# Optimization experiments

Measured on AMD Instinct MI355X. Metric: run time of the kernel, lower is better.

The kernel has to match this reference:

```python
import jax, jax.numpy as jnp
import numpy as np

B, L, V, D = 8, 2048, 1024, 512  # batch, seq (max_len), vocab_size (input feat), embedding_dim

def setup_inputs() -> dict:
    key = jax.random.key(0)
    kx, kq, kk, kv = jax.random.split(key, 4)
    scale = 1.0 / np.sqrt(V)
    return {
        "x": jax.random.normal(kx, (B, L, V), dtype=jnp.float32),
        "Wq": jax.random.uniform(kq, (D, V), dtype=jnp.float32, minval=-scale, maxval=scale),
        "Wk": jax.random.uniform(kk, (D, V), dtype=jnp.float32, minval=-scale, maxval=scale),
        "Wv": jax.random.uniform(kv, (D, V), dtype=jnp.float32, minval=-scale, maxval=scale),
    }

def reference(x, Wq, Wk, Wv):
    # nn.Linear without bias: y = x @ W.T
    q = jnp.einsum('blv,dv->bld', x, Wq)
    k = jnp.einsum('blv,dv->bld', x, Wk)
    v = jnp.einsum('blv,dv->bld', x, Wv)
    scores = jnp.einsum('bqd,bkd->bqk', q, k) / jnp.sqrt(jnp.float32(D))
    attn = jax.nn.softmax(scores, axis=2)
    return jnp.einsum('bqk,bkd->bqd', attn, v)
```

## Files before the change

### kernel.cpp

```cpp
#include <hip/hip_runtime.h>
#include <cstdint>
#include <cstddef>


typedef __attribute__((ext_vector_type(8))) __bf16 bf16x8;
typedef __attribute__((ext_vector_type(4))) float f32x4;
typedef __attribute__((ext_vector_type(4))) unsigned short ushort4v;
typedef __attribute__((ext_vector_type(4))) unsigned int uint4v;

__device__ __forceinline__ unsigned short f2bf(float f) {
  unsigned u = __float_as_uint(f);
  return (unsigned short)((u + 0x7fffu + ((u >> 16) & 1u)) >> 16);
}

__device__ __forceinline__ void async_load16(const unsigned short* g, unsigned short* l) {
  __builtin_amdgcn_global_load_lds(
      (__attribute__((address_space(1))) void*)(g),
      (__attribute__((address_space(3))) void*)(l), 16, 0, 0);
}

__global__ __launch_bounds__(256) void cvt_all(
    const float* __restrict__ x, const float* __restrict__ Wq,
    const float* __restrict__ Wk, const float* __restrict__ Wv,
    unsigned short* __restrict__ xb, unsigned short* __restrict__ wf) {
  int u0 = blockIdx.x, tid = threadIdx.x;
  const float* src;
  unsigned short* dst;
  int i;
  if (u0 < 16384) {
    i = (u0 * 256 + tid) * 4;
    src = x; dst = xb;
  } else {
    int bx = u0 - 16384;
    src = (bx < 512) ? Wq : (bx < 1024) ? Wk : Wv;
    int seg = (bx < 512) ? 0 : (bx < 1024) ? 1 : 2;
    i = ((bx & 511) * 256 + tid) * 4;
    dst = wf + seg * 524288;
  }
  float4 v = *(const float4*)(src + i);
  ushort4v o;
  o.x = f2bf(v.x); o.y = f2bf(v.y); o.z = f2bf(v.z); o.w = f2bf(v.w);
  *(ushort4v*)(dst + i) = o;
}

template <int NT, bool RSUM>
__device__ __forceinline__ void core8p(
    const unsigned short* __restrict__ A, const unsigned short* __restrict__ B,
    int ldA, int ldB, unsigned short* smem, int tid,
    f32x4 (&acc)[4][4], float (&rsum)[4]) {
  const int lane = tid & 63, wid = tid >> 6;
  const int wm = wid & 3, wn = wid >> 2;
  const int cl = lane & 15, g = lane >> 4;
  const int r0 = tid >> 3;
  const int cs8 = ((tid & 7) ^ (r0 & 7)) * 8;

  #pragma unroll
  for (int p = 0; p < 4; ++p)
    async_load16(&A[(size_t)(p * 64 + r0) * ldA + cs8], &smem[(p * 512 + tid) * 8]);
  #pragma unroll
  for (int p = 0; p < 2; ++p)
    async_load16(&B[(size_t)(p * 64 + r0) * ldB + cs8], &smem[16384 + (p * 512 + tid) * 8]);
  #pragma unroll
  for (int p = 0; p < 4; ++p)
    async_load16(&A[(size_t)(p * 64 + r0) * ldA + 64 + cs8], &smem[24576 + (p * 512 + tid) * 8]);
  #pragma unroll
  for (int p = 0; p < 2; ++p)
    async_load16(&B[(size_t)(p * 64 + r0) * ldB + 64 + cs8], &smem[40960 + (p * 512 + tid) * 8]);
  asm volatile("s_waitcnt vmcnt(6)" ::: "memory");
  __builtin_amdgcn_s_barrier();

  int cur = 0;
  for (int t = 0; t < NT; ++t) {
    unsigned short* bufc = smem + cur * 24576;
    int nb = cur + 2; if (nb >= 3) nb -= 3;
    unsigned short* bufn = smem + nb * 24576;
    const bool st = (t + 2 < NT);
    const int k2 = (t + 2) * 64;

    #pragma unroll
    for (int kh = 0; kh < 2; ++kh) {
      bf16x8 a4[4], b4[4];
      #pragma unroll
      for (int mt = 0; mt < 4; ++mt) {
        int rr = wm * 64 + mt * 16 + cl;
        a4[mt] = *(const bf16x8*)&bufc[(rr * 8 + ((kh * 4 + g) ^ (rr & 7))) * 8];
      }
      #pragma unroll
      for (int nt = 0; nt < 4; ++nt) {
        int rr = wn * 64 + nt * 16 + cl;
        b4[nt] = *(const bf16x8*)&bufc[16384 + (rr * 8 + ((kh * 4 + g) ^ (rr & 7))) * 8];
      }
      if (kh == 0) {
        if (st) {
          #pragma unroll
          for (int p = 0; p < 4; ++p)
            async_load16(&A[(size_t)(p * 64 + r0) * ldA + k2 + cs8],
                         &bufn[(p * 512 + tid) * 8]);
        }
      } else {
        if (st) {
          #pragma unroll
          for (int p = 0; p < 2; ++p)
            async_load16(&B[(size_t)(p * 64 + r0) * ldB + k2 + cs8],
                         &bufn[16384 + (p * 512 + tid) * 8]);
          asm volatile("s_waitcnt vmcnt(6)" ::: "memory");
        } else if (t + 1 < NT) {
          asm volatile("s_waitcnt vmcnt(0)" ::: "memory");
        }
      }
      __builtin_amdgcn_s_barrier();
      asm volatile("s_waitcnt lgkmcnt(0)" ::: "memory");
      __builtin_amdgcn_sched_barrier(0);
      if (RSUM) {
        #pragma unroll
        for (int nt = 0; nt < 4; ++nt) {
          uint4v u = __builtin_bit_cast(uint4v, b4[nt]);
          #pragma unroll
          for (int q = 0; q < 4; ++q)
            rsum[nt] += __uint_as_float(u[q] << 16) +
                        __uint_as_float(u[q] & 0xffff0000u);
        }
      }
      __builtin_amdgcn_s_setprio(1);
      #pragma unroll
      for (int mt = 0; mt < 4; ++mt)
        #pragma unroll
        for (int nt = 0; nt < 4; ++nt)
          acc[mt][nt] = __builtin_amdgcn_mfma_f32_16x16x32_bf16(
              a4[mt], b4[nt], acc[mt][nt], 0, 0, 0);
      __builtin_amdgcn_s_setprio(0);
      __builtin_amdgcn_s_barrier();
    }
    cur = cur + 1; if (cur == 3) cur = 0;
  }
}

__global__ __launch_bounds__(512, 2) void gemm_qkv8(
    const unsigned short* __restrict__ A0,
    const unsigned short* __restrict__ Bw,
    unsigned short* __restrict__ qk,
    unsigned short* __restrict__ vT) {
  extern __shared__ __align__(16) unsigned short smem[];
  const int tid = threadIdx.x;
  int flat = blockIdx.x;
  int sub = flat >> 3;
  int bxp = sub % 12;
  int byp = (flat & 7) * 8 + sub / 12;
  const unsigned short* A = A0 + (size_t)byp * 256 * 1024;
  const unsigned short* B = Bw + (size_t)bxp * 128 * 1024;

  f32x4 acc[4][4] = {};
  float rsum[4];
  core8p<16, false>(A, B, 1024, 1024, smem, tid, acc, rsum);

  const int lane = tid & 63, wid = tid >> 6;
  const int wm = wid & 3, wn = wid >> 2, cl = lane & 15, g = lane >> 4;

  if (bxp < 8) {
    unsigned short* Cc = qk + (size_t)byp * 256 * 1024 + (size_t)bxp * 128;
    #pragma unroll
    for (int mt = 0; mt < 4; ++mt)
      #pragma unroll
      for (int nt = 0; nt < 4; ++nt) {
        int col = wn * 64 + nt * 16 + cl;
        int row0 = wm * 64 + mt * 16 + g * 4;
        #pragma unroll
        for (int j = 0; j < 4; ++j)
          Cc[(size_t)(row0 + j) * 1024 + col] = f2bf(acc[mt][nt][j]);
      }
  } else {
    int nvx = bxp - 8;
    #pragma unroll
    for (int mt = 0; mt < 4; ++mt)
      #pragma unroll
      for (int nt = 0; nt < 4; ++nt) {
        int d = nvx * 128 + wn * 64 + nt * 16 + cl;
        int grow0 = byp * 256 + wm * 64 + mt * 16 + g * 4;
        int b = grow0 >> 11, l0 = grow0 & 2047;
        ushort4v o;
        o.x = f2bf(acc[mt][nt][0]); o.y = f2bf(acc[mt][nt][1]);
        o.z = f2bf(acc[mt][nt][2]); o.w = f2bf(acc[mt][nt][3]);
        *(ushort4v*)&vT[(size_t)b * 1048576 + (size_t)d * 2048 + l0] = o;
      }
  }
}

__global__ __launch_bounds__(512, 2) void gemm_pvT8(
    const unsigned short* __restrict__ S, const unsigned short* __restrict__ vT,
    float* __restrict__ out) {
  extern __shared__ __align__(16) unsigned short smem[];
  const int tid = threadIdx.x;
  int flat = blockIdx.x;
  int b = flat & 7, rem = flat >> 3;
  int dblk = rem & 1, qblk = rem >> 1;
  const unsigned short* A  = vT + (size_t)b * 1048576 + (size_t)dblk * 256 * 2048;
  const unsigned short* Bs = S  + (size_t)b * 4194304 + (size_t)qblk * 128 * 2048;

  f32x4 acc[4][4] = {};
  float rsum[4] = {0.f, 0.f, 0.f, 0.f};
  core8p<32, true>(A, Bs, 2048, 2048, smem, tid, acc, rsum);

  const int lane = tid & 63, wid = tid >> 6;
  const int wm = wid & 3, wn = wid >> 2, cl = lane & 15, g = lane >> 4;

  #pragma unroll
  for (int nt = 0; nt < 4; ++nt) {
    float v = rsum[nt];
    v += __shfl_xor(v, 16, 64);
    v += __shfl_xor(v, 32, 64);
    rsum[nt] = v;
  }

  #pragma unroll
  for (int nt = 0; nt < 4; ++nt) {
    float inv = __builtin_amdgcn_rcpf(rsum[nt]);
    int qpos = qblk * 128 + wn * 64 + nt * 16 + cl;
    #pragma unroll
    for (int mt = 0; mt < 4; ++mt) {
      int d0 = dblk * 256 + wm * 64 + mt * 16 + g * 4;
      float* op = out + ((size_t)b * 2048 + qpos) * 512 + d0;
      float4 o;
      o.x = acc[mt][nt][0] * inv;
      o.y = acc[mt][nt][1] * inv;
      o.z = acc[mt][nt][2] * inv;
      o.w = acc[mt][nt][3] * inv;
      *(float4*)op = o;
    }
  }
}

__global__ __launch_bounds__(256) void gemm_exp(
    const unsigned short* __restrict__ qk,
    unsigned short* __restrict__ S) {
  const float scale = 0.044194173824159216f;
  __shared__ unsigned short sA[128 * 64];
  __shared__ unsigned short sB[128 * 64];
  const int tid = threadIdx.x;
  const int lane = tid & 63, wid = tid >> 6;
  const int wm = wid & 1, wn = wid >> 1;
  const int cl = lane & 15, g = lane >> 4;

  int flat = blockIdx.x + (blockIdx.y << 4) + (blockIdx.z << 8);
  int z = flat & 7, rem = flat >> 3;
  int bxp = rem & 15, byp = rem >> 4;

  const unsigned short* A  = qk + (size_t)z * 2097152 + (size_t)byp * 128 * 1024;
  const unsigned short* Bk = qk + 512 + (size_t)z * 2097152 + (size_t)bxp * 128 * 1024;

  f32x4 acc[4][4] = {};

  for (int k0 = 0; k0 < 512; k0 += 64) {
    __syncthreads();
    #pragma unroll
    for (int p = 0; p < 4; ++p) {
      int u = p * 256 + tid;
      int r = u >> 3, cs = (u & 7) ^ (r & 7);
      async_load16(&A[(size_t)r * 1024 + k0 + cs * 8], &sA[u * 8]);
      async_load16(&Bk[(size_t)r * 1024 + k0 + cs * 8], &sB[u * 8]);
    }
    __syncthreads();

    bf16x8 aF[4][2], bF[4][2];
    #pragma unroll
    for (int t = 0; t < 4; ++t)
      #pragma unroll
      for (int kh = 0; kh < 2; ++kh) {
        int ra = wm * 64 + t * 16 + cl;
        aF[t][kh] = *(const bf16x8*)&sA[(ra * 8 + ((kh * 4 + g) ^ (ra & 7))) * 8];
        int rb = wn * 64 + t * 16 + cl;
        bF[t][kh] = *(const bf16x8*)&sB[(rb * 8 + ((kh * 4 + g) ^ (rb & 7))) * 8];
      }
    #pragma unroll
    for (int mt = 0; mt < 4; ++mt)
      #pragma unroll
      for (int nt = 0; nt < 4; ++nt)
        #pragma unroll
        for (int kh = 0; kh < 2; ++kh)
          acc[mt][nt] = __builtin_amdgcn_mfma_f32_16x16x32_bf16(
              aF[mt][kh], bF[nt][kh], acc[mt][nt], 0, 0, 0);
  }

  unsigned short* Cc = S + (size_t)z * 4194304 +
                       (size_t)byp * 128 * 2048 + (size_t)bxp * 128;
  #pragma unroll
  for (int mt = 0; mt < 4; ++mt)
    #pragma unroll
    for (int nt = 0; nt < 4; ++nt) {
      int col = wn * 64 + nt * 16 + cl;
      int row0 = wm * 64 + mt * 16 + g * 4;
      #pragma unroll
      for (int j = 0; j < 4; ++j)
        Cc[(size_t)(row0 + j) * 2048 + col] =
            f2bf(__expf(acc[mt][nt][j] * scale));
    }
}

extern "C" void kernel_launch(void* const* d_in, const int* in_sizes, int n_in,
                              void* d_out, int out_size, void* d_ws, size_t ws_size,
                              hipStream_t stream) {
  const float* x  = (const float*)d_in[0];
  const float* Wq = (const float*)d_in[1];
  const float* Wk = (const float*)d_in[2];
  const float* Wv = (const float*)d_in[3];
  float* out = (float*)d_out;
  char* ws = (char*)d_ws;

  unsigned short* xb = (unsigned short*)ws;
  unsigned short* S  = (unsigned short*)ws;
  unsigned short* wf = (unsigned short*)(ws + 33554432);
  unsigned short* qk = (unsigned short*)(ws + 67108864);
  unsigned short* vT = (unsigned short*)(ws + 100663296);

  static bool inited = false;
  if (!inited) {
    hipFuncSetAttribute((const void*)gemm_qkv8,
                        hipFuncAttributeMaxDynamicSharedMemorySize, 147456);
    hipFuncSetAttribute((const void*)gemm_pvT8,
                        hipFuncAttributeMaxDynamicSharedMemorySize, 147456);
    inited = true;
  }

  hipLaunchKernelGGL(cvt_all, dim3(17920), dim3(256), 0, stream,
                     x, Wq, Wk, Wv, xb, wf);

  hipLaunchKernelGGL(gemm_qkv8, dim3(768), dim3(512), 147456, stream,
                     xb, wf, qk, vT);

  hipLaunchKernelGGL(gemm_exp, dim3(16, 16, 8), dim3(256), 0, stream, qk, S);

  hipLaunchKernelGGL(gemm_pvT8, dim3(256), dim3(512), 147456, stream,
                     S, vT, out);

  (void)in_sizes; (void)n_in; (void)out_size; (void)ws_size;
}
```

Baseline: 268.3 us.

## Rewrite QKV GEMM with 4-wave blocks and larger per-wave tiles; grid-stride convert

Replaces the 8-wave shared core QKV projection GEMM with a dedicated 4-wave kernel in which each wave computes a 128x64 tile (8x4 MFMAs). Loads are triple-buffered with explicit vmcnt/lgkmcnt waits and sched barriers. The aim is more MFMA work per LDS fragment read and less cross-wave synchronisation. The fp32-to-bf16 convert kernel becomes grid-stride over 2048 blocks instead of launching 17920. The cost is higher register pressure at one block per CU with 144KB of LDS, which leaves fewer waves to hide latency.

```diff
diff --git a/kernel.cpp b/kernel.cpp
--- a/kernel.cpp
+++ b/kernel.cpp
@@ -23,24 +23,149 @@
     const float* __restrict__ x, const float* __restrict__ Wq,
     const float* __restrict__ Wk, const float* __restrict__ Wv,
     unsigned short* __restrict__ xb, unsigned short* __restrict__ wf) {
-  int u0 = blockIdx.x, tid = threadIdx.x;
-  const float* src;
-  unsigned short* dst;
-  int i;
-  if (u0 < 16384) {
-    i = (u0 * 256 + tid) * 4;
-    src = x; dst = xb;
+  int tid = threadIdx.x;
+  for (int u0 = blockIdx.x; u0 < 17920; u0 += 2048) {
+    const float* src;
+    unsigned short* dst;
+    int i;
+    if (u0 < 16384) {
+      i = (u0 * 256 + tid) * 4;
+      src = x; dst = xb;
+    } else {
+      int bx = u0 - 16384;
+      src = (bx < 512) ? Wq : (bx < 1024) ? Wk : Wv;
+      int seg = (bx < 512) ? 0 : (bx < 1024) ? 1 : 2;
+      i = ((bx & 511) * 256 + tid) * 4;
+      dst = wf + seg * 524288;
+    }
+    float4 v = *(const float4*)(src + i);
+    ushort4v o;
+    o.x = f2bf(v.x); o.y = f2bf(v.y); o.z = f2bf(v.z); o.w = f2bf(v.w);
+    *(ushort4v*)(dst + i) = o;
+  }
+}
+
+__global__ __launch_bounds__(256, 1) void gemm_qkv4(
+    const unsigned short* __restrict__ A0,
+    const unsigned short* __restrict__ Bw,
+    unsigned short* __restrict__ qk,
+    unsigned short* __restrict__ vT) {
+  extern __shared__ __align__(16) unsigned short smem[];
+  const int tid = threadIdx.x;
+  const int lane = tid & 63, wid = tid >> 6;
+  const int wm = wid & 1, wn = wid >> 1;
+  const int cl = lane & 15, g = lane >> 4;
+  const int r0 = tid >> 3;
+  const int cs8 = ((tid & 7) ^ (r0 & 7)) * 8;
+
+  int flat = blockIdx.x;
+  int sub = flat >> 3;
+  int bxp = sub % 12;
+  int byp = (flat & 7) * 8 + sub / 12;
+
+  const unsigned short* A = A0 + (size_t)byp * 256 * 1024;
+  const unsigned short* B = Bw + (size_t)bxp * 128 * 1024;
+
+  f32x4 acc[8][4] = {};
+
+  #pragma unroll
+  for (int p = 0; p < 8; ++p)
+    async_load16(&A[(size_t)(p * 32 + r0) * 1024 + cs8], &smem[(p * 256 + tid) * 8]);
+  #pragma unroll
+  for (int p = 0; p < 4; ++p)
+    async_load16(&B[(size_t)(p * 32 + r0) * 1024 + cs8], &smem[16384 + (p * 256 + tid) * 8]);
+  #pragma unroll
+  for (int p = 0; p < 8; ++p)
+    async_load16(&A[(size_t)(p * 32 + r0) * 1024 + 64 + cs8], &smem[24576 + (p * 256 + tid) * 8]);
+  #pragma unroll
+  for (int p = 0; p < 4; ++p)
+    async_load16(&B[(size_t)(p * 32 + r0) * 1024 + 64 + cs8], &smem[40960 + (p * 256 + tid) * 8]);
+  asm volatile("s_waitcnt vmcnt(12)" ::: "memory");
+  __builtin_amdgcn_s_barrier();
+
+  int cur = 0;
+  const int NT = 16;
+  for (int t = 0; t < NT; ++t) {
+    unsigned short* bufc = smem + cur * 24576;
+    int nb = cur + 2; if (nb >= 3) nb -= 3;
+    unsigned short* bufn = smem + nb * 24576;
+    const bool st = (t + 2 < NT);
+    const int k2 = (t + 2) * 64;
+
+    #pragma unroll
+    for (int kh = 0; kh < 2; ++kh) {
+      bf16x8 a8[8], b4[4];
+      #pragma unroll
+      for (int mt = 0; mt < 8; ++mt) {
+        int rr = wm * 128 + mt * 16 + cl;
+        a8[mt] = *(const bf16x8*)&bufc[(rr * 8 + ((kh * 4 + g) ^ (rr & 7))) * 8];
+      }
+      #pragma unroll
+      for (int nt = 0; nt < 4; ++nt) {
+        int rr = wn * 64 + nt * 16 + cl;
+        b4[nt] = *(const bf16x8*)&bufc[16384 + (rr * 8 + ((kh * 4 + g) ^ (rr & 7))) * 8];
+      }
+      if (kh == 0) {
+        if (st) {
+          #pragma unroll
+          for (int p = 0; p < 8; ++p)
+            async_load16(&A[(size_t)(p * 32 + r0) * 1024 + k2 + cs8],
+                         &bufn[(p * 256 + tid) * 8]);
+        }
+      } else {
+        if (st) {
+          #pragma unroll
+          for (int p = 0; p < 4; ++p)
+            async_load16(&B[(size_t)(p * 32 + r0) * 1024 + k2 + cs8],
+                         &bufn[16384 + (p * 256 + tid) * 8]);
+          asm volatile("s_waitcnt vmcnt(12)" ::: "memory");
+        } else if (t + 1 < NT) {
+          asm volatile("s_waitcnt vmcnt(0)" ::: "memory");
+        }
+      }
+      __builtin_amdgcn_s_barrier();
+      asm volatile("s_waitcnt lgkmcnt(0)" ::: "memory");
+      __builtin_amdgcn_sched_barrier(0);
+      __builtin_amdgcn_s_setprio(1);
+      #pragma unroll
+      for (int mt = 0; mt < 8; ++mt)
+        #pragma unroll
+        for (int nt = 0; nt < 4; ++nt)
+          acc[mt][nt] = __builtin_amdgcn_mfma_f32_16x16x32_bf16(
+              a8[mt], b4[nt], acc[mt][nt], 0, 0, 0);
+      __builtin_amdgcn_s_setprio(0);
+      __builtin_amdgcn_s_barrier();
+    }
+    cur = cur + 1; if (cur == 3) cur = 0;
+  }
+
+  if (bxp < 8) {
+    unsigned short* Cc = qk + (size_t)byp * 256 * 1024 + (size_t)bxp * 128;
+    #pragma unroll
+    for (int mt = 0; mt < 8; ++mt)
+      #pragma unroll
+      for (int nt = 0; nt < 4; ++nt) {
+        int col = wn * 64 + nt * 16 + cl;
+        int row0 = wm * 128 + mt * 16 + g * 4;
+        #pragma unroll
+        for (int j = 0; j < 4; ++j)
+          Cc[(size_t)(row0 + j) * 1024 + col] = f2bf(acc[mt][nt][j]);
+      }
   } else {
-    int bx = u0 - 16384;
-    src = (bx < 512) ? Wq : (bx < 1024) ? Wk : Wv;
-    int seg = (bx < 512) ? 0 : (bx < 1024) ? 1 : 2;
-    i = ((bx & 511) * 256 + tid) * 4;
-    dst = wf + seg * 524288;
-  }
-  float4 v = *(const float4*)(src + i);
-  ushort4v o;
-  o.x = f2bf(v.x); o.y = f2bf(v.y); o.z = f2bf(v.z); o.w = f2bf(v.w);
-  *(ushort4v*)(dst + i) = o;
+    int nvx = bxp - 8;
+    #pragma unroll
+    for (int mt = 0; mt < 8; ++mt)
+      #pragma unroll
+      for (int nt = 0; nt < 4; ++nt) {
+        int d = nvx * 128 + wn * 64 + nt * 16 + cl;
+        int grow0 = byp * 256 + wm * 128 + mt * 16 + g * 4;
+        int b = grow0 >> 11, l0 = grow0 & 2047;
+        ushort4v o;
+        o.x = f2bf(acc[mt][nt][0]); o.y = f2bf(acc[mt][nt][1]);
+        o.z = f2bf(acc[mt][nt][2]); o.w = f2bf(acc[mt][nt][3]);
+        *(ushort4v*)&vT[(size_t)b * 1048576 + (size_t)d * 2048 + l0] = o;
+      }
+  }
 }
 
 template <int NT, bool RSUM>
@@ -135,56 +260,6 @@
   }
 }
 
-__global__ __launch_bounds__(512, 2) void gemm_qkv8(
-    const unsigned short* __restrict__ A0,
-    const unsigned short* __restrict__ Bw,
-    unsigned short* __restrict__ qk,
-    unsigned short* __restrict__ vT) {
-  extern __shared__ __align__(16) unsigned short smem[];
-  const int tid = threadIdx.x;
-  int flat = blockIdx.x;
-  int sub = flat >> 3;
-  int bxp = sub % 12;
-  int byp = (flat & 7) * 8 + sub / 12;
-  const unsigned short* A = A0 + (size_t)byp * 256 * 1024;
-  const unsigned short* B = Bw + (size_t)bxp * 128 * 1024;
-
-  f32x4 acc[4][4] = {};
-  float rsum[4];
-  core8p<16, false>(A, B, 1024, 1024, smem, tid, acc, rsum);
-
-  const int lane = tid & 63, wid = tid >> 6;
-  const int wm = wid & 3, wn = wid >> 2, cl = lane & 15, g = lane >> 4;
-
-  if (bxp < 8) {
-    unsigned short* Cc = qk + (size_t)byp * 256 * 1024 + (size_t)bxp * 128;
-    #pragma unroll
-    for (int mt = 0; mt < 4; ++mt)
-      #pragma unroll
-      for (int nt = 0; nt < 4; ++nt) {
-        int col = wn * 64 + nt * 16 + cl;
-        int row0 = wm * 64 + mt * 16 + g * 4;
-        #pragma unroll
-        for (int j = 0; j < 4; ++j)
-          Cc[(size_t)(row0 + j) * 1024 + col] = f2bf(acc[mt][nt][j]);
-      }
-  } else {
-    int nvx = bxp - 8;
-    #pragma unroll
-    for (int mt = 0; mt < 4; ++mt)
-      #pragma unroll
-      for (int nt = 0; nt < 4; ++nt) {
-        int d = nvx * 128 + wn * 64 + nt * 16 + cl;
-        int grow0 = byp * 256 + wm * 64 + mt * 16 + g * 4;
-        int b = grow0 >> 11, l0 = grow0 & 2047;
-        ushort4v o;
-        o.x = f2bf(acc[mt][nt][0]); o.y = f2bf(acc[mt][nt][1]);
-        o.z = f2bf(acc[mt][nt][2]); o.w = f2bf(acc[mt][nt][3]);
-        *(ushort4v*)&vT[(size_t)b * 1048576 + (size_t)d * 2048 + l0] = o;
-      }
-  }
-}
-
 __global__ __launch_bounds__(512, 2) void gemm_pvT8(
     const unsigned short* __restrict__ S, const unsigned short* __restrict__ vT,
     float* __restrict__ out) {
@@ -313,17 +388,17 @@
 
   static bool inited = false;
   if (!inited) {
-    hipFuncSetAttribute((const void*)gemm_qkv8,
+    hipFuncSetAttribute((const void*)gemm_qkv4,
                         hipFuncAttributeMaxDynamicSharedMemorySize, 147456);
     hipFuncSetAttribute((const void*)gemm_pvT8,
                         hipFuncAttributeMaxDynamicSharedMemorySize, 147456);
     inited = true;
   }
 
-  hipLaunchKernelGGL(cvt_all, dim3(17920), dim3(256), 0, stream,
+  hipLaunchKernelGGL(cvt_all, dim3(2048), dim3(256), 0, stream,
                      x, Wq, Wk, Wv, xb, wf);
 
-  hipLaunchKernelGGL(gemm_qkv8, dim3(768), dim3(512), 147456, stream,
+  hipLaunchKernelGGL(gemm_qkv4, dim3(768), dim3(256), 147456, stream,
                      xb, wf, qk, vT);
 
   hipLaunchKernelGGL(gemm_exp, dim3(16, 16, 8), dim3(256), 0, stream, qk, S);
```

Result: slower. 282.6 us (+5.3%).

## Replace P·V kernel with 128x128-tile grid and grid-stride the conversion kernel

Applied to the files above, without the earlier changes.

Replaces the large 512-thread, triple-buffered transposed P·V kernel (256 blocks of 256x128 tiles) with a simpler 256-thread kernel that uses 128x128 tiles over P rows and V columns. That doubles the block count to 512 so more of the GPU's compute units get work. Row sums for the softmax normalisation are now taken from the A fragments and reduced through shared memory. The catch is that the new kernel is single-buffered with two barriers per k-step, so load and compute no longer overlap. Separately, the fp32-to-bf16 conversion kernel now launches a fixed 2048 blocks that loop over the work in a grid-stride pattern, instead of one block per chunk.

```diff
diff --git a/kernel.cpp b/kernel.cpp
--- a/kernel.cpp
+++ b/kernel.cpp
@@ -23,31 +23,32 @@
     const float* __restrict__ x, const float* __restrict__ Wq,
     const float* __restrict__ Wk, const float* __restrict__ Wv,
     unsigned short* __restrict__ xb, unsigned short* __restrict__ wf) {
-  int u0 = blockIdx.x, tid = threadIdx.x;
-  const float* src;
-  unsigned short* dst;
-  int i;
-  if (u0 < 16384) {
-    i = (u0 * 256 + tid) * 4;
-    src = x; dst = xb;
-  } else {
-    int bx = u0 - 16384;
-    src = (bx < 512) ? Wq : (bx < 1024) ? Wk : Wv;
-    int seg = (bx < 512) ? 0 : (bx < 1024) ? 1 : 2;
-    i = ((bx & 511) * 256 + tid) * 4;
-    dst = wf + seg * 524288;
-  }
-  float4 v = *(const float4*)(src + i);
-  ushort4v o;
-  o.x = f2bf(v.x); o.y = f2bf(v.y); o.z = f2bf(v.z); o.w = f2bf(v.w);
-  *(ushort4v*)(dst + i) = o;
-}
-
-template <int NT, bool RSUM>
+  int tid = threadIdx.x;
+  for (int u0 = blockIdx.x; u0 < 17920; u0 += 2048) {
+    const float* src;
+    unsigned short* dst;
+    int i;
+    if (u0 < 16384) {
+      i = (u0 * 256 + tid) * 4;
+      src = x; dst = xb;
+    } else {
+      int bx = u0 - 16384;
+      src = (bx < 512) ? Wq : (bx < 1024) ? Wk : Wv;
+      int seg = (bx < 512) ? 0 : (bx < 1024) ? 1 : 2;
+      i = ((bx & 511) * 256 + tid) * 4;
+      dst = wf + seg * 524288;
+    }
+    float4 v = *(const float4*)(src + i);
+    ushort4v o;
+    o.x = f2bf(v.x); o.y = f2bf(v.y); o.z = f2bf(v.z); o.w = f2bf(v.w);
+    *(ushort4v*)(dst + i) = o;
+  }
+}
+
+template <int NT>
 __device__ __forceinline__ void core8p(
     const unsigned short* __restrict__ A, const unsigned short* __restrict__ B,
-    int ldA, int ldB, unsigned short* smem, int tid,
-    f32x4 (&acc)[4][4], float (&rsum)[4]) {
+    int ldA, int ldB, unsigned short* smem, int tid, f32x4 (&acc)[4][4]) {
   const int lane = tid & 63, wid = tid >> 6;
   const int wm = wid & 3, wn = wid >> 2;
   const int cl = lane & 15, g = lane >> 4;
@@ -111,16 +112,6 @@
       __builtin_amdgcn_s_barrier();
       asm volatile("s_waitcnt lgkmcnt(0)" ::: "memory");
       __builtin_amdgcn_sched_barrier(0);
-      if (RSUM) {
-        #pragma unroll
-        for (int nt = 0; nt < 4; ++nt) {
-          uint4v u = __builtin_bit_cast(uint4v, b4[nt]);
-          #pragma unroll
-          for (int q = 0; q < 4; ++q)
-            rsum[nt] += __uint_as_float(u[q] << 16) +
-                        __uint_as_float(u[q] & 0xffff0000u);
-        }
-      }
       __builtin_amdgcn_s_setprio(1);
       #pragma unroll
       for (int mt = 0; mt < 4; ++mt)
@@ -150,8 +141,7 @@
   const unsigned short* B = Bw + (size_t)bxp * 128 * 1024;
 
   f32x4 acc[4][4] = {};
-  float rsum[4];
-  core8p<16, false>(A, B, 1024, 1024, smem, tid, acc, rsum);
+  core8p<16>(A, B, 1024, 1024, smem, tid, acc);
 
   const int lane = tid & 63, wid = tid >> 6;
   const int wm = wid & 3, wn = wid >> 2, cl = lane & 15, g = lane >> 4;
@@ -182,50 +172,6 @@
         o.z = f2bf(acc[mt][nt][2]); o.w = f2bf(acc[mt][nt][3]);
         *(ushort4v*)&vT[(size_t)b * 1048576 + (size_t)d * 2048 + l0] = o;
       }
-  }
-}
-
-__global__ __launch_bounds__(512, 2) void gemm_pvT8(
-    const unsigned short* __restrict__ S, const unsigned short* __restrict__ vT,
-    float* __restrict__ out) {
-  extern __shared__ __align__(16) unsigned short smem[];
-  const int tid = threadIdx.x;
-  int flat = blockIdx.x;
-  int b = flat & 7, rem = flat >> 3;
-  int dblk = rem & 1, qblk = rem >> 1;
-  const unsigned short* A  = vT + (size_t)b * 1048576 + (size_t)dblk * 256 * 2048;
-  const unsigned short* Bs = S  + (size_t)b * 4194304 + (size_t)qblk * 128 * 2048;
-
-  f32x4 acc[4][4] = {};
-  float rsum[4] = {0.f, 0.f, 0.f, 0.f};
-  core8p<32, true>(A, Bs, 2048, 2048, smem, tid, acc, rsum);
-
-  const int lane = tid & 63, wid = tid >> 6;
-  const int wm = wid & 3, wn = wid >> 2, cl = lane & 15, g = lane >> 4;
-
-  #pragma unroll
-  for (int nt = 0; nt < 4; ++nt) {
-    float v = rsum[nt];
-    v += __shfl_xor(v, 16, 64);
-    v += __shfl_xor(v, 32, 64);
-    rsum[nt] = v;
-  }
-
-  #pragma unroll
-  for (int nt = 0; nt < 4; ++nt) {
-    float inv = __builtin_amdgcn_rcpf(rsum[nt]);
-    int qpos = qblk * 128 + wn * 64 + nt * 16 + cl;
-    #pragma unroll
-    for (int mt = 0; mt < 4; ++mt) {
-      int d0 = dblk * 256 + wm * 64 + mt * 16 + g * 4;
-      float* op = out + ((size_t)b * 2048 + qpos) * 512 + d0;
-      float4 o;
-      o.x = acc[mt][nt][0] * inv;
-      o.y = acc[mt][nt][1] * inv;
-      o.z = acc[mt][nt][2] * inv;
-      o.w = acc[mt][nt][3] * inv;
-      *(float4*)op = o;
-    }
   }
 }
 
@@ -295,6 +241,95 @@
     }
 }
 
+__global__ __launch_bounds__(256) void gemm_pv(
+    const unsigned short* __restrict__ P, const unsigned short* __restrict__ vT,
+    float* __restrict__ out) {
+  __shared__ unsigned short sA[128 * 64];
+  __shared__ unsigned short sB[128 * 64];
+  __shared__ float rs[128];
+  const int tid = threadIdx.x;
+  const int lane = tid & 63, wid = tid >> 6;
+  const int wm = wid & 1, wn = wid >> 1;
+  const int cl = lane & 15, g = lane >> 4;
+
+  int flat = blockIdx.x + (blockIdx.y << 2) + (blockIdx.z << 6);
+  int z = flat & 7, rem = flat >> 3;
+  int bxp = rem & 3, byp = rem >> 2;
+
+  const int m0 = byp * 128, n0 = bxp * 128;
+  const unsigned short* A  = P + (size_t)z * 4194304 + (size_t)m0 * 2048;
+  const unsigned short* Bv = vT + (size_t)z * 1048576 + (size_t)n0 * 2048;
+
+  f32x4 acc[4][4] = {};
+  float rsum[4] = {0.f, 0.f, 0.f, 0.f};
+
+  for (int k0 = 0; k0 < 2048; k0 += 64) {
+    __syncthreads();
+    #pragma unroll
+    for (int p = 0; p < 4; ++p) {
+      int u = p * 256 + tid;
+      int r = u >> 3, cs = (u & 7) ^ (r & 7);
+      async_load16(&A[(size_t)r * 2048 + k0 + cs * 8], &sA[u * 8]);
+      async_load16(&Bv[(size_t)r * 2048 + k0 + cs * 8], &sB[u * 8]);
+    }
+    __syncthreads();
+
+    bf16x8 aF[4][2], bF[4][2];
+    #pragma unroll
+    for (int t = 0; t < 4; ++t)
+      #pragma unroll
+      for (int kh = 0; kh < 2; ++kh) {
+        int ra = wm * 64 + t * 16 + cl;
+        aF[t][kh] = *(const bf16x8*)&sA[(ra * 8 + ((kh * 4 + g) ^ (ra & 7))) * 8];
+        int rb = wn * 64 + t * 16 + cl;
+        bF[t][kh] = *(const bf16x8*)&sB[(rb * 8 + ((kh * 4 + g) ^ (rb & 7))) * 8];
+      }
+    #pragma unroll
+    for (int t = 0; t < 4; ++t)
+      #pragma unroll
+      for (int kh = 0; kh < 2; ++kh) {
+        uint4v u = __builtin_bit_cast(uint4v, aF[t][kh]);
+        #pragma unroll
+        for (int q = 0; q < 4; ++q)
+          rsum[t] += __uint_as_float(u[q] << 16) +
+                     __uint_as_float(u[q] & 0xffff0000u);
+      }
+    #pragma unroll
+    for (int mt = 0; mt < 4; ++mt)
+      #pragma unroll
+      for (int nt = 0; nt < 4; ++nt)
+        #pragma unroll
+        for (int kh = 0; kh < 2; ++kh)
+          acc[mt][nt] = __builtin_amdgcn_mfma_f32_16x16x32_bf16(
+              aF[mt][kh], bF[nt][kh], acc[mt][nt], 0, 0, 0);
+  }
+
+  #pragma unroll
+  for (int mt = 0; mt < 4; ++mt) {
+    float v = rsum[mt];
+    v += __shfl_xor(v, 16, 64);
+    v += __shfl_xor(v, 32, 64);
+    if (wn == 0 && lane < 16) rs[wm * 64 + mt * 16 + lane] = v;
+  }
+  __syncthreads();
+
+  #pragma unroll
+  for (int mt = 0; mt < 4; ++mt) {
+    int row0l = wm * 64 + mt * 16 + g * 4;
+    float inv[4];
+    #pragma unroll
+    for (int j = 0; j < 4; ++j) inv[j] = __builtin_amdgcn_rcpf(rs[row0l + j]);
+    #pragma unroll
+    for (int nt = 0; nt < 4; ++nt) {
+      int col = n0 + wn * 64 + nt * 16 + cl;
+      float* op = out + ((size_t)z * 2048 + m0 + row0l) * 512 + col;
+      #pragma unroll
+      for (int j = 0; j < 4; ++j)
+        op[(size_t)j * 512] = acc[mt][nt][j] * inv[j];
+    }
+  }
+}
+
 extern "C" void kernel_launch(void* const* d_in, const int* in_sizes, int n_in,
                               void* d_out, int out_size, void* d_ws, size_t ws_size,
                               hipStream_t stream) {
@@ -315,12 +350,10 @@
   if (!inited) {
     hipFuncSetAttribute((const void*)gemm_qkv8,
                         hipFuncAttributeMaxDynamicSharedMemorySize, 147456);
-    hipFuncSetAttribute((const void*)gemm_pvT8,
-                        hipFuncAttributeMaxDynamicSharedMemorySize, 147456);
     inited = true;
   }
 
-  hipLaunchKernelGGL(cvt_all, dim3(17920), dim3(256), 0, stream,
+  hipLaunchKernelGGL(cvt_all, dim3(2048), dim3(256), 0, stream,
                      x, Wq, Wk, Wv, xb, wf);
 
   hipLaunchKernelGGL(gemm_qkv8, dim3(768), dim3(512), 147456, stream,
@@ -328,8 +361,7 @@
 
   hipLaunchKernelGGL(gemm_exp, dim3(16, 16, 8), dim3(256), 0, stream, qk, S);
 
-  hipLaunchKernelGGL(gemm_pvT8, dim3(256), dim3(512), 147456, stream,
-                     S, vT, out);
+  hipLaunchKernelGGL(gemm_pv, dim3(4, 16, 8), dim3(256), 0, stream, S, vT, out);
 
   (void)in_sizes; (void)n_in; (void)out_size; (void)ws_size;
 }
```

Result: faster. 251.2 us (-6.4%).

## Move QK^T exp onto pipelined 256x128 core and reorient PV GEMM

Applied to the files above, without the earlier changes.

Replaces the simple single-buffered QK^T+exp kernel with one built on the shared multi-stage async-load core8p, using 256x128 tiles and 512 threads. The PV GEMM is reoriented so P is the A operand, with row sums taken from A fragments and shared through LDS for normalization. The conversion kernel becomes grid-stride with fewer blocks. The aim is better latency hiding and MFMA utilization in the score GEMM, at the cost of extra LDS for the row sums and scalar fp32 output stores.

```diff
diff --git a/kernel.cpp b/kernel.cpp
--- a/kernel.cpp
+++ b/kernel.cpp
@@ -23,24 +23,26 @@
     const float* __restrict__ x, const float* __restrict__ Wq,
     const float* __restrict__ Wk, const float* __restrict__ Wv,
     unsigned short* __restrict__ xb, unsigned short* __restrict__ wf) {
-  int u0 = blockIdx.x, tid = threadIdx.x;
-  const float* src;
-  unsigned short* dst;
-  int i;
-  if (u0 < 16384) {
-    i = (u0 * 256 + tid) * 4;
-    src = x; dst = xb;
-  } else {
-    int bx = u0 - 16384;
-    src = (bx < 512) ? Wq : (bx < 1024) ? Wk : Wv;
-    int seg = (bx < 512) ? 0 : (bx < 1024) ? 1 : 2;
-    i = ((bx & 511) * 256 + tid) * 4;
-    dst = wf + seg * 524288;
-  }
-  float4 v = *(const float4*)(src + i);
-  ushort4v o;
-  o.x = f2bf(v.x); o.y = f2bf(v.y); o.z = f2bf(v.z); o.w = f2bf(v.w);
-  *(ushort4v*)(dst + i) = o;
+  int tid = threadIdx.x;
+  for (int u0 = blockIdx.x; u0 < 17920; u0 += 2048) {
+    const float* src;
+    unsigned short* dst;
+    int i;
+    if (u0 < 16384) {
+      i = (u0 * 256 + tid) * 4;
+      src = x; dst = xb;
+    } else {
+      int bx = u0 - 16384;
+      src = (bx < 512) ? Wq : (bx < 1024) ? Wk : Wv;
+      int seg = (bx < 512) ? 0 : (bx < 1024) ? 1 : 2;
+      i = ((bx & 511) * 256 + tid) * 4;
+      dst = wf + seg * 524288;
+    }
+    float4 v = *(const float4*)(src + i);
+    ushort4v o;
+    o.x = f2bf(v.x); o.y = f2bf(v.y); o.z = f2bf(v.z); o.w = f2bf(v.w);
+    *(ushort4v*)(dst + i) = o;
+  }
 }
 
 template <int NT, bool RSUM>
@@ -113,11 +115,11 @@
       __builtin_amdgcn_sched_barrier(0);
       if (RSUM) {
         #pragma unroll
-        for (int nt = 0; nt < 4; ++nt) {
-          uint4v u = __builtin_bit_cast(uint4v, b4[nt]);
+        for (int mt = 0; mt < 4; ++mt) {
+          uint4v u = __builtin_bit_cast(uint4v, a4[mt]);
           #pragma unroll
           for (int q = 0; q < 4; ++q)
-            rsum[nt] += __uint_as_float(u[q] << 16) +
+            rsum[mt] += __uint_as_float(u[q] << 16) +
                         __uint_as_float(u[q] & 0xffff0000u);
         }
       }
@@ -185,114 +187,86 @@
   }
 }
 
-__global__ __launch_bounds__(512, 2) void gemm_pvT8(
-    const unsigned short* __restrict__ S, const unsigned short* __restrict__ vT,
+__global__ __launch_bounds__(512, 2) void gemm_exp8(
+    const unsigned short* __restrict__ qk,
+    unsigned short* __restrict__ S) {
+  const float scale = 0.044194173824159216f;
+  extern __shared__ __align__(16) unsigned short smem[];
+  const int tid = threadIdx.x;
+  int flat = blockIdx.x;
+  int z = flat & 7, rem = flat >> 3;
+  int bxp = rem & 15, byp = rem >> 4;
+
+  const unsigned short* A  = qk + (size_t)z * 2097152 + (size_t)byp * 256 * 1024;
+  const unsigned short* Bk = qk + 512 + (size_t)z * 2097152 + (size_t)bxp * 128 * 1024;
+
+  f32x4 acc[4][4] = {};
+  float rsum[4];
+  core8p<8, false>(A, Bk, 1024, 1024, smem, tid, acc, rsum);
+
+  const int lane = tid & 63, wid = tid >> 6;
+  const int wm = wid & 3, wn = wid >> 2, cl = lane & 15, g = lane >> 4;
+
+  unsigned short* Cc = S + (size_t)z * 4194304 +
+                       (size_t)byp * 256 * 2048 + (size_t)bxp * 128;
+  #pragma unroll
+  for (int mt = 0; mt < 4; ++mt)
+    #pragma unroll
+    for (int nt = 0; nt < 4; ++nt) {
+      int col = wn * 64 + nt * 16 + cl;
+      int row0 = wm * 64 + mt * 16 + g * 4;
+      #pragma unroll
+      for (int j = 0; j < 4; ++j)
+        Cc[(size_t)(row0 + j) * 2048 + col] =
+            f2bf(__expf(acc[mt][nt][j] * scale));
+    }
+}
+
+__global__ __launch_bounds__(512, 2) void gemm_pv8(
+    const unsigned short* __restrict__ P, const unsigned short* __restrict__ vT,
     float* __restrict__ out) {
   extern __shared__ __align__(16) unsigned short smem[];
   const int tid = threadIdx.x;
   int flat = blockIdx.x;
-  int b = flat & 7, rem = flat >> 3;
-  int dblk = rem & 1, qblk = rem >> 1;
-  const unsigned short* A  = vT + (size_t)b * 1048576 + (size_t)dblk * 256 * 2048;
-  const unsigned short* Bs = S  + (size_t)b * 4194304 + (size_t)qblk * 128 * 2048;
+  int z = flat & 7, rem = flat >> 3;
+  int bxp = rem & 3, byp = rem >> 2;
+
+  const int m0 = byp * 256, n0 = bxp * 128;
+  const unsigned short* A  = P + (size_t)z * 4194304 + (size_t)m0 * 2048;
+  const unsigned short* Bv = vT + (size_t)z * 1048576 + (size_t)n0 * 2048;
 
   f32x4 acc[4][4] = {};
   float rsum[4] = {0.f, 0.f, 0.f, 0.f};
-  core8p<32, true>(A, Bs, 2048, 2048, smem, tid, acc, rsum);
+  core8p<32, true>(A, Bv, 2048, 2048, smem, tid, acc, rsum);
 
   const int lane = tid & 63, wid = tid >> 6;
   const int wm = wid & 3, wn = wid >> 2, cl = lane & 15, g = lane >> 4;
 
-  #pragma unroll
-  for (int nt = 0; nt < 4; ++nt) {
-    float v = rsum[nt];
+  float* rs = (float*)(smem + 73728);
+  #pragma unroll
+  for (int mt = 0; mt < 4; ++mt) {
+    float v = rsum[mt];
     v += __shfl_xor(v, 16, 64);
     v += __shfl_xor(v, 32, 64);
-    rsum[nt] = v;
-  }
-
-  #pragma unroll
-  for (int nt = 0; nt < 4; ++nt) {
-    float inv = __builtin_amdgcn_rcpf(rsum[nt]);
-    int qpos = qblk * 128 + wn * 64 + nt * 16 + cl;
-    #pragma unroll
-    for (int mt = 0; mt < 4; ++mt) {
-      int d0 = dblk * 256 + wm * 64 + mt * 16 + g * 4;
-      float* op = out + ((size_t)b * 2048 + qpos) * 512 + d0;
-      float4 o;
-      o.x = acc[mt][nt][0] * inv;
-      o.y = acc[mt][nt][1] * inv;
-      o.z = acc[mt][nt][2] * inv;
-      o.w = acc[mt][nt][3] * inv;
-      *(float4*)op = o;
+    if (wn == 0 && lane < 16) rs[wm * 64 + mt * 16 + lane] = v;
+  }
+  __syncthreads();
+
+  #pragma unroll
+  for (int mt = 0; mt < 4; ++mt) {
+    int row0 = wm * 64 + mt * 16 + g * 4;
+    float inv[4];
+    #pragma unroll
+    for (int j = 0; j < 4; ++j) inv[j] = __builtin_amdgcn_rcpf(rs[row0 + j]);
+    #pragma unroll
+    for (int nt = 0; nt < 4; ++nt) {
+      int col = n0 + wn * 64 + nt * 16 + cl;
+      float* op = out + ((size_t)z * 2048 + m0 + row0) * 512 + col;
+      #pragma unroll
+      for (int j = 0; j < 4; ++j)
+        op[(size_t)j * 512] = acc[mt][nt][j] * inv[j];
     }
   }
-}
-
-__global__ __launch_bounds__(256) void gemm_exp(
-    const unsigned short* __restrict__ qk,
-    unsigned short* __restrict__ S) {
-  const float scale = 0.044194173824159216f;
-  __shared__ unsigned short sA[128 * 64];
-  __shared__ unsigned short sB[128 * 64];
-  const int tid = threadIdx.x;
-  const int lane = tid & 63, wid = tid >> 6;
-  const int wm = wid & 1, wn = wid >> 1;
-  const int cl = lane & 15, g = lane >> 4;
-
-  int flat = blockIdx.x + (blockIdx.y << 4) + (blockIdx.z << 8);
-  int z = flat & 7, rem = flat >> 3;
-  int bxp = rem & 15, byp = rem >> 4;
-
-  const unsigned short* A  = qk + (size_t)z * 2097152 + (size_t)byp * 128 * 1024;
-  const unsigned short* Bk = qk + 512 + (size_t)z * 2097152 + (size_t)bxp * 128 * 1024;
-
-  f32x4 acc[4][4] = {};
-
-  for (int k0 = 0; k0 < 512; k0 += 64) {
-    __syncthreads();
-    #pragma unroll
-    for (int p = 0; p < 4; ++p) {
-      int u = p * 256 + tid;
-      int r = u >> 3, cs = (u & 7) ^ (r & 7);
-      async_load16(&A[(size_t)r * 1024 + k0 + cs * 8], &sA[u * 8]);
-      async_load16(&Bk[(size_t)r * 1024 + k0 + cs * 8], &sB[u * 8]);
-    }
-    __syncthreads();
-
-    bf16x8 aF[4][2], bF[4][2];
-    #pragma unroll
-    for (int t = 0; t < 4; ++t)
-      #pragma unroll
-      for (int kh = 0; kh < 2; ++kh) {
-        int ra = wm * 64 + t * 16 + cl;
-        aF[t][kh] = *(const bf16x8*)&sA[(ra * 8 + ((kh * 4 + g) ^ (ra & 7))) * 8];
-        int rb = wn * 64 + t * 16 + cl;
-        bF[t][kh] = *(const bf16x8*)&sB[(rb * 8 + ((kh * 4 + g) ^ (rb & 7))) * 8];
-      }
-    #pragma unroll
-    for (int mt = 0; mt < 4; ++mt)
-      #pragma unroll
-      for (int nt = 0; nt < 4; ++nt)
-        #pragma unroll
-        for (int kh = 0; kh < 2; ++kh)
-          acc[mt][nt] = __builtin_amdgcn_mfma_f32_16x16x32_bf16(
-              aF[mt][kh], bF[nt][kh], acc[mt][nt], 0, 0, 0);
-  }
-
-  unsigned short* Cc = S + (size_t)z * 4194304 +
-                       (size_t)byp * 128 * 2048 + (size_t)bxp * 128;
-  #pragma unroll
-  for (int mt = 0; mt < 4; ++mt)
-    #pragma unroll
-    for (int nt = 0; nt < 4; ++nt) {
-      int col = wn * 64 + nt * 16 + cl;
-      int row0 = wm * 64 + mt * 16 + g * 4;
-      #pragma unroll
-      for (int j = 0; j < 4; ++j)
-        Cc[(size_t)(row0 + j) * 2048 + col] =
-            f2bf(__expf(acc[mt][nt][j] * scale));
-    }
 }
 
 extern "C" void kernel_launch(void* const* d_in, const int* in_sizes, int n_in,
@@ -315,20 +289,22 @@
   if (!inited) {
     hipFuncSetAttribute((const void*)gemm_qkv8,
                         hipFuncAttributeMaxDynamicSharedMemorySize, 147456);
-    hipFuncSetAttribute((const void*)gemm_pvT8,
+    hipFuncSetAttribute((const void*)gemm_exp8,
                         hipFuncAttributeMaxDynamicSharedMemorySize, 147456);
+    hipFuncSetAttribute((const void*)gemm_pv8,
+                        hipFuncAttributeMaxDynamicSharedMemorySize, 148480);
     inited = true;
   }
 
-  hipLaunchKernelGGL(cvt_all, dim3(17920), dim3(256), 0, stream,
+  hipLaunchKernelGGL(cvt_all, dim3(2048), dim3(256), 0, stream,
                      x, Wq, Wk, Wv, xb, wf);
 
   hipLaunchKernelGGL(gemm_qkv8, dim3(768), dim3(512), 147456, stream,
                      xb, wf, qk, vT);
 
-  hipLaunchKernelGGL(gemm_exp, dim3(16, 16, 8), dim3(256), 0, stream, qk, S);
-
-  hipLaunchKernelGGL(gemm_pvT8, dim3(256), dim3(512), 147456, stream,
+  hipLaunchKernelGGL(gemm_exp8, dim3(1024), dim3(512), 147456, stream, qk, S);
+
+  hipLaunchKernelGGL(gemm_pv8, dim3(256), dim3(512), 148480, stream,
                      S, vT, out);
 
   (void)in_sizes; (void)n_in; (void)out_size; (void)ws_size;
```

Result: no change. 273.1 us (+1.8%).
